# Kernel tuning notes

Hardware: AMD Instinct MI355X
Metric: run time of the kernel (lower is better)

## Reference

```python
import jax, jax.numpy as jnp
import numpy as np

B, T, D, H = 256, 256, 64, 512  # batch, seq_len, input_dim, hidden_dim


def setup_inputs() -> dict:
    key = jax.random.key(0)
    ks = jax.random.split(key, 12)
    scale = 0.05
    inp = {"x": jax.random.normal(ks[0], (B, T, D), dtype=jnp.float32)}
    in_dims = [D, H, H]
    for i in range(3):
        inp[f"Wx{i}"] = jax.random.normal(ks[1 + 3 * i], (in_dims[i], H), dtype=jnp.float32) * scale
        inp[f"Wh{i}"] = jax.random.normal(ks[2 + 3 * i], (H, H), dtype=jnp.float32) * scale
        inp[f"b{i}"] = jnp.zeros((H,), dtype=jnp.float32)
    inp["Wf"] = jax.random.normal(ks[10], (H, 1), dtype=jnp.float32) * scale
    inp["bf"] = jnp.zeros((1,), dtype=jnp.float32)
    return inp


def _rnn_seq(x, Wx, Wh, b):
    """SimpleRNN with return_sequences=True. x: [B,T,Din] -> [B,T,H].
    Keras eval mode: dropout inactive. h_t = tanh(x_t Wx + h_{t-1} Wh + b)."""
    # Precompute input projection for all steps (one big GEMM).
    xp = jnp.einsum('btd,dh->bth', x, Wx) + b  # [B,T,H]

    def step(h, xt):
        h2 = jnp.tanh(xt + h @ Wh)
        return h2, h2

    h0 = jnp.zeros((x.shape[0], Wh.shape[0]), dtype=x.dtype)
    _, ys = jax.lax.scan(step, h0, jnp.swapaxes(xp, 0, 1))  # ys: [T,B,H]
    return jnp.swapaxes(ys, 0, 1)


def _rnn_last(x, Wx, Wh, b):
    """SimpleRNN with return_sequences=False. x: [B,T,Din] -> [B,H] (final state)."""
    xp = jnp.einsum('btd,dh->bth', x, Wx) + b

    def step(h, xt):
        h2 = jnp.tanh(xt + h @ Wh)
        return h2, None

    h0 = jnp.zeros((x.shape[0], Wh.shape[0]), dtype=x.dtype)
    hT, _ = jax.lax.scan(step, h0, jnp.swapaxes(xp, 0, 1))
    return hT


def reference(x, Wx0, Wh0, b0, Wx1, Wh1, b1, Wx2, Wh2, b2, Wf, bf):
    h = _rnn_seq(x, Wx0, Wh0, b0)   # [B,T,H]
    h = _rnn_seq(h, Wx1, Wh1, b1)   # [B,T,H]
    h = _rnn_last(h, Wx2, Wh2, b2)  # [B,H]
    return h @ Wf + bf              # [B,1]
```

## Files before the change

kernel.cpp:

```cpp
#include <hip/hip_runtime.h>


typedef unsigned short u16;
typedef unsigned int   u32;
typedef unsigned long long u64;

typedef __attribute__((ext_vector_type(8))) short short8;
typedef __attribute__((ext_vector_type(4))) float f32x4;
typedef __attribute__((ext_vector_type(4))) int   i32x4;

#define N_B 256
#define N_T 256
#define N_D 64
#define N_H 512
#define LAY 3
#define BG  8
#define CGS 8
#define ROWS 32
#define WCOL 64
#define NWG (LAY * BG * CGS)
#define CNT_TGT 8
#define CPAD 16
#define CNT_LINES (LAY * BG * N_T)
#define XBASE ((CNT_LINES + 2 * BG) * CPAD)
#define XCCS  (XBASE + CPAD)
#define CNT_U32 (XCCS + NWG)
#define SPIN_LIM (1u << 22)

__device__ __forceinline__ u16 f2bf(float f) {
  union { float f; u32 u; } v; v.f = f;
  u32 u = v.u;
  u += 0x7fffu + ((u >> 16) & 1u);
  return (u16)(u >> 16);
}
__device__ __forceinline__ float bf2f(u16 h) {
  union { u32 u; float f; } v; v.u = ((u32)h) << 16;
  return v.f;
}
__device__ __forceinline__ short8 ld8(const u16* p) { return *(const short8*)p; }
__device__ __forceinline__ short8 cvt8(const float* p) {
  short8 r;
#pragma unroll
  for (int j = 0; j < 8; ++j) r[j] = (short)f2bf(p[j]);
  return r;
}
__device__ __forceinline__ short8 as_s8(i32x4 v) {
  union { i32x4 i; short8 s; } u; u.i = v; return u.s;
}
__device__ __forceinline__ float fast_tanh(float x) {
  float xc = fminf(fmaxf(x, -9.f), 9.f);
  float e  = __builtin_amdgcn_exp2f(xc * 2.8853900817779268f);
  return 1.f - 2.f * __builtin_amdgcn_rcpf(e + 1.f);
}
__device__ __forceinline__ u32 rmw_read(u32* p) {
  u32 v, z = 0;
  asm volatile("global_atomic_add %0, %1, %2, off sc0\n\ts_waitcnt vmcnt(0)"
               : "=v"(v) : "v"(p), "v"(z) : "memory");
  return v;
}
__device__ __forceinline__ void poll_cnt(u32* cp, u32 target, bool fast, bool* dead) {
  u32 it = 0;
  for (;;) {
    u32 v = fast ? rmw_read(cp)
                 : __hip_atomic_load(cp, __ATOMIC_RELAXED, __HIP_MEMORY_SCOPE_AGENT);
    if (v >= target) return;
    if (it >= 2) __builtin_amdgcn_s_sleep(1);
    if (++it > SPIN_LIM) { *dead = true; return; }
  }
}
__device__ __forceinline__ void lds_set(volatile u32* f, u32 v) {
  __hip_atomic_store((u32*)f, v, __ATOMIC_RELEASE, __HIP_MEMORY_SCOPE_WORKGROUP);
}
__device__ __forceinline__ void lds_wait(volatile u32* f, u32 want, bool* dead) {
  u32 it = 0;
  while (__hip_atomic_load((u32*)f, __ATOMIC_ACQUIRE, __HIP_MEMORY_SCOPE_WORKGROUP) != want) {
    if (++it > SPIN_LIM) { *dead = true; return; }
  }
}

__device__ __forceinline__ void load16_async_fast(const u16* p, i32x4 f[16]) {
  asm volatile(
      "global_load_dwordx4 %0, %16, off sc0\n\t"
      "global_load_dwordx4 %1, %16, off offset:64 sc0\n\t"
      "global_load_dwordx4 %2, %16, off offset:128 sc0\n\t"
      "global_load_dwordx4 %3, %16, off offset:192 sc0\n\t"
      "global_load_dwordx4 %4, %16, off offset:256 sc0\n\t"
      "global_load_dwordx4 %5, %16, off offset:320 sc0\n\t"
      "global_load_dwordx4 %6, %16, off offset:384 sc0\n\t"
      "global_load_dwordx4 %7, %16, off offset:448 sc0\n\t"
      "global_load_dwordx4 %8, %16, off offset:512 sc0\n\t"
      "global_load_dwordx4 %9, %16, off offset:576 sc0\n\t"
      "global_load_dwordx4 %10, %16, off offset:640 sc0\n\t"
      "global_load_dwordx4 %11, %16, off offset:704 sc0\n\t"
      "global_load_dwordx4 %12, %16, off offset:768 sc0\n\t"
      "global_load_dwordx4 %13, %16, off offset:832 sc0\n\t"
      "global_load_dwordx4 %14, %16, off offset:896 sc0\n\t"
      "global_load_dwordx4 %15, %16, off offset:960 sc0"
      : "=&v"(f[0]), "=&v"(f[1]), "=&v"(f[2]), "=&v"(f[3]),
        "=&v"(f[4]), "=&v"(f[5]), "=&v"(f[6]), "=&v"(f[7]),
        "=&v"(f[8]), "=&v"(f[9]), "=&v"(f[10]), "=&v"(f[11]),
        "=&v"(f[12]), "=&v"(f[13]), "=&v"(f[14]), "=&v"(f[15])
      : "v"(p) : "memory");
}
__device__ __forceinline__ void load16_async_slow(const u16* p, i32x4 f[16]) {
  asm volatile(
      "global_load_dwordx4 %0, %16, off sc0 sc1\n\t"
      "global_load_dwordx4 %1, %16, off offset:64 sc0 sc1\n\t"
      "global_load_dwordx4 %2, %16, off offset:128 sc0 sc1\n\t"
      "global_load_dwordx4 %3, %16, off offset:192 sc0 sc1\n\t"
      "global_load_dwordx4 %4, %16, off offset:256 sc0 sc1\n\t"
      "global_load_dwordx4 %5, %16, off offset:320 sc0 sc1\n\t"
      "global_load_dwordx4 %6, %16, off offset:384 sc0 sc1\n\t"
      "global_load_dwordx4 %7, %16, off offset:448 sc0 sc1\n\t"
      "global_load_dwordx4 %8, %16, off offset:512 sc0 sc1\n\t"
      "global_load_dwordx4 %9, %16, off offset:576 sc0 sc1\n\t"
      "global_load_dwordx4 %10, %16, off offset:640 sc0 sc1\n\t"
      "global_load_dwordx4 %11, %16, off offset:704 sc0 sc1\n\t"
      "global_load_dwordx4 %12, %16, off offset:768 sc0 sc1\n\t"
      "global_load_dwordx4 %13, %16, off offset:832 sc0 sc1\n\t"
      "global_load_dwordx4 %14, %16, off offset:896 sc0 sc1\n\t"
      "global_load_dwordx4 %15, %16, off offset:960 sc0 sc1"
      : "=&v"(f[0]), "=&v"(f[1]), "=&v"(f[2]), "=&v"(f[3]),
        "=&v"(f[4]), "=&v"(f[5]), "=&v"(f[6]), "=&v"(f[7]),
        "=&v"(f[8]), "=&v"(f[9]), "=&v"(f[10]), "=&v"(f[11]),
        "=&v"(f[12]), "=&v"(f[13]), "=&v"(f[14]), "=&v"(f[15])
      : "v"(p) : "memory");
}

#define MFMA16(a, b, c) __builtin_amdgcn_mfma_f32_16x16x32_bf16((a), (b), (c), 0, 0, 0)

#define STEPK(kt, N)                                                        \
  do {                                                                      \
    asm volatile("s_waitcnt vmcnt(" #N ")" : "+v"(fr[kt]) :: "memory");     \
    short8 a_ = as_s8(fr[kt]);                                              \
    acc[0] = MFMA16(a_, wf[kt][0], acc[0]);                                 \
    acc[1] = MFMA16(a_, wf[kt][1], acc[1]);                                 \
    acc[2] = MFMA16(a_, wf[kt][2], acc[2]);                                 \
    acc[3] = MFMA16(a_, wf[kt][3], acc[3]);                                 \
  } while (0)
#define K16_PIPE()                                                          \
  STEPK(0, 15); STEPK(1, 14); STEPK(2, 13); STEPK(3, 12);                   \
  STEPK(4, 11); STEPK(5, 10); STEPK(6, 9);  STEPK(7, 8);                    \
  STEPK(8, 7);  STEPK(9, 6);  STEPK(10, 5); STEPK(11, 4);                   \
  STEPK(12, 3); STEPK(13, 2); STEPK(14, 1); STEPK(15, 0)

__global__ __launch_bounds__(256, 1)
void rnn_pipe(const float* __restrict__ x,
              const float* __restrict__ Wx0, const float* __restrict__ Wh0, const float* __restrict__ b0,
              const float* __restrict__ Wx1, const float* __restrict__ Wh1, const float* __restrict__ b1,
              const float* __restrict__ Wx2, const float* __restrict__ Wh2, const float* __restrict__ b2,
              u16* __restrict__ seq0, u16* __restrict__ seq1, u16* __restrict__ seq2,
              u32* __restrict__ cnt) {
  const int tid  = threadIdx.x;
  const int lane = tid & 63;
  const int w    = tid >> 6;
  const int quad = lane >> 4;
  const int l16  = lane & 15;
  const int half = w & 1;
  const bool is_rec = (w < 2);

  __shared__ u16   WhT[WCOL][N_H];
  __shared__ u16   WxT[WCOL][N_H];
  __shared__ float Cbuf[2][ROWS][WCOL + 1];
  __shared__ u32   sflags[6];
  __shared__ u32   sx[NWG];
  __shared__ u32   sbar;

  u32* arrive = cnt + XBASE;
  u32* xccs   = cnt + XCCS;

  u32 xcc;
  asm volatile("s_getreg_b32 %0, hwreg(HW_REG_XCC_ID)" : "=s"(xcc));
  if (tid == 0) {
    u32* xe = xccs + blockIdx.x;
    u32 xv = xcc & 7u;
    asm volatile("global_store_dword %0, %1, off sc0 sc1\n\ts_waitcnt vmcnt(0)"
                 :: "v"(xe), "v"(xv) : "memory");
    __hip_atomic_fetch_add(arrive, 1u, __ATOMIC_RELAXED, __HIP_MEMORY_SCOPE_AGENT);
    u32 it = 0; u32 bd = 0;
    while (rmw_read(arrive) < (u32)NWG) {
      __builtin_amdgcn_s_sleep(1);
      if (++it > SPIN_LIM) { bd = 1; break; }
    }
    sbar = bd;
  }
  if (tid < 6) sflags[tid] = 0;
  __syncthreads();
  const bool bar_dead = (sbar != 0);
  if (!bar_dead && tid < NWG) sx[tid] = rmw_read(xccs + tid) & 7u;
  __syncthreads();

  int bg, layer, j; bool fast;
  if (bar_dead) {
    bg = blockIdx.x & 7;
    int rst = blockIdx.x >> 3;
    layer = rst >> 3; j = rst & 7;
    fast = false;
  } else {
    u64 c64 = 0;
    int myrid = -1, mypend = -1, pends = 0;
    for (int i = 0; i < NWG; ++i) {
      u32 xv = sx[i];
      u32 c = (u32)((c64 >> (8u * xv)) & 0xffu);
      if (c < 24u) {
        if (i == (int)blockIdx.x) myrid = (int)(xv * 24u + c);
        c64 += (1ull << (8u * xv));
      } else {
        if (i == (int)blockIdx.x) mypend = pends;
        ++pends;
      }
    }
    if (myrid < 0) {
      int p = 0;
      for (int xb = 0; xb < 8; ++xb) {
        u32 c = (u32)((c64 >> (8u * xb)) & 0xffu);
        for (u32 s = c; s < 24u; ++s) {
          if (p == mypend) myrid = xb * 24 + (int)s;
          ++p;
        }
      }
    }
    bg = myrid / 24;
    int slot = myrid % 24;
    layer = slot >> 3; j = slot & 7;
    fast = (((c64 >> (8u * (u32)bg)) & 0xffu) >= 24u);
  }
  const int b = bg;

  const float *Wx, *Wh, *bias; const u16 *in_seq = nullptr; u16 *out_seq;
  if (layer == 0)      { Wx = Wx0; Wh = Wh0; bias = b0; out_seq = seq0; }
  else if (layer == 1) { Wx = Wx1; Wh = Wh1; bias = b1; in_seq = seq0; out_seq = seq1; }
  else                 { Wx = Wx2; Wh = Wh2; bias = b2; in_seq = seq1; out_seq = seq2; }
  const int kin = (layer == 0) ? N_D : N_H;
  u32* cnt_own  = cnt + (size_t)(layer * BG + b) * N_T * CPAD;
  u32* cnt_prev = (layer > 0) ? cnt + (size_t)((layer - 1) * BG + b) * N_T * CPAD : nullptr;

  for (int e = tid; e < WCOL * N_H; e += 256) {
    int n = e & 63, k = e >> 6;
    WhT[n][(k + 8 * n) & (N_H - 1)] = f2bf(Wh[k * N_H + j * WCOL + n]);
  }
  for (int e = tid; e < WCOL * kin; e += 256) {
    int n = e & 63, k = e >> 6;
    WxT[n][(k + 8 * n) & (kin - 1)] = f2bf(Wx[k * N_H + j * WCOL + n]);
  }
  float bv[4];
#pragma unroll
  for (int n = 0; n < 4; ++n) bv[n] = bias[j * WCOL + n * 16 + l16];
  __syncthreads();

  short8 wf[16][4];
  if (is_rec) {
#pragma unroll
    for (int kt = 0; kt < 16; ++kt)
#pragma unroll
      for (int n = 0; n < 4; ++n) {
        int nl = n * 16 + l16;
        wf[kt][n] = ld8(&WhT[nl][(kt * 32 + quad * 8 + 8 * nl) & (N_H - 1)]);
      }
  } else if (layer == 0) {
#pragma unroll
    for (int n = 0; n < 4; ++n) {
      int nl = n * 16 + l16;
      wf[0][n] = ld8(&WxT[nl][(quad * 8 + 8 * nl) & (N_D - 1)]);
      wf[1][n] = ld8(&WxT[nl][(32 + quad * 8 + 8 * nl) & (N_D - 1)]);
    }
  } else {
#pragma unroll
    for (int kt = 0; kt < 16; ++kt)
#pragma unroll
      for (int n = 0; n < 4; ++n) {
        int nl = n * 16 + l16;
        wf[kt][n] = ld8(&WxT[nl][(kt * 32 + quad * 8 + 8 * nl) & (N_H - 1)]);
      }
  }

  const int arow = b * ROWS + half * 16 + l16;
  bool dead = false;

  for (int t = 0; t < N_T; ++t) {
    const int par = t & 1;
    f32x4 acc[4] = {{0.f,0.f,0.f,0.f},{0.f,0.f,0.f,0.f},{0.f,0.f,0.f,0.f},{0.f,0.f,0.f,0.f}};

    if (!is_rec) {
      if (layer == 0) {
        const float* xp = x + ((size_t)arow * N_T + t) * N_D + quad * 8;
        short8 f0 = cvt8(xp), f1 = cvt8(xp + 32);
#pragma unroll
        for (int n = 0; n < 4; ++n) {
          acc[n] = MFMA16(f0, wf[0][n], acc[n]);
          acc[n] = MFMA16(f1, wf[1][n], acc[n]);
        }
      } else {
        if (half == 0) {
          if (lane == 0) {
            if (!dead) poll_cnt(cnt_prev + (size_t)t * CPAD, CNT_TGT, fast, &dead);
            lds_set(&sflags[2 + par], (u32)(t + 1));
          }
        } else {
          if (lane == 0 && !dead) lds_wait(&sflags[2 + par], (u32)(t + 1), &dead);
        }
        const u16* sp = in_seq + ((size_t)t * N_B + arow) * N_H + quad * 8;
        i32x4 fr[16];
        if (fast) load16_async_fast(sp, fr);
        else      load16_async_slow(sp, fr);
        K16_PIPE();
      }
      int rb = half * 16 + quad * 4;
#pragma unroll
      for (int n = 0; n < 4; ++n)
#pragma unroll
        for (int r = 0; r < 4; ++r)
          Cbuf[par][rb + r][n * 16 + l16] = acc[n][r];
    } else {
      if (t > 0) {
        if (half == 0) {
          if (lane == 0) {
            if (!dead) poll_cnt(cnt_own + (size_t)(t - 1) * CPAD, CNT_TGT, fast, &dead);
            lds_set(&sflags[par], (u32)t);
          }
        } else {
          if (lane == 0 && !dead) lds_wait(&sflags[par], (u32)t, &dead);
        }
        const u16* ap = out_seq + ((size_t)(t - 1) * N_B + arow) * N_H + quad * 8;
        i32x4 fr[16];
        if (fast) load16_async_fast(ap, fr);
        else      load16_async_slow(ap, fr);
        K16_PIPE();
      }
    }

    __syncthreads();

    if (is_rec) {
      int rb = half * 16 + quad * 4;
      u32 hv[4][4];
#pragma unroll
      for (int n = 0; n < 4; ++n)
#pragma unroll
        for (int r = 0; r < 4; ++r)
          hv[n][r] = (u32)f2bf(fast_tanh(acc[n][r] + Cbuf[par][rb + r][n * 16 + l16] + bv[n]));
      u16* hdst = out_seq + ((size_t)t * N_B + b * ROWS + half * 16 + quad * 4) * N_H
                  + j * WCOL + l16;
      if (fast) {
        asm volatile(
            "global_store_short %0, %1, off sc0\n\t"
            "global_store_short %0, %2, off offset:1024 sc0\n\t"
            "global_store_short %0, %3, off offset:2048 sc0\n\t"
            "global_store_short %0, %4, off offset:3072 sc0\n\t"
            "global_store_short %0, %5, off offset:32 sc0\n\t"
            "global_store_short %0, %6, off offset:1056 sc0\n\t"
            "global_store_short %0, %7, off offset:2080 sc0\n\t"
            "global_store_short %0, %8, off offset:3104 sc0\n\t"
            "global_store_short %0, %9, off offset:64 sc0\n\t"
            "global_store_short %0, %10, off offset:1088 sc0\n\t"
            "global_store_short %0, %11, off offset:2112 sc0\n\t"
            "global_store_short %0, %12, off offset:3136 sc0\n\t"
            "global_store_short %0, %13, off offset:96 sc0\n\t"
            "global_store_short %0, %14, off offset:1120 sc0\n\t"
            "global_store_short %0, %15, off offset:2144 sc0\n\t"
            "global_store_short %0, %16, off offset:3168 sc0"
            :: "v"(hdst),
               "v"(hv[0][0]), "v"(hv[0][1]), "v"(hv[0][2]), "v"(hv[0][3]),
               "v"(hv[1][0]), "v"(hv[1][1]), "v"(hv[1][2]), "v"(hv[1][3]),
               "v"(hv[2][0]), "v"(hv[2][1]), "v"(hv[2][2]), "v"(hv[2][3]),
               "v"(hv[3][0]), "v"(hv[3][1]), "v"(hv[3][2]), "v"(hv[3][3])
            : "memory");
      } else {
        asm volatile(
            "global_store_short %0, %1, off sc0 sc1\n\t"
            "global_store_short %0, %2, off offset:1024 sc0 sc1\n\t"
            "global_store_short %0, %3, off offset:2048 sc0 sc1\n\t"
            "global_store_short %0, %4, off offset:3072 sc0 sc1\n\t"
            "global_store_short %0, %5, off offset:32 sc0 sc1\n\t"
            "global_store_short %0, %6, off offset:1056 sc0 sc1\n\t"
            "global_store_short %0, %7, off offset:2080 sc0 sc1\n\t"
            "global_store_short %0, %8, off offset:3104 sc0 sc1\n\t"
            "global_store_short %0, %9, off offset:64 sc0 sc1\n\t"
            "global_store_short %0, %10, off offset:1088 sc0 sc1\n\t"
            "global_store_short %0, %11, off offset:2112 sc0 sc1\n\t"
            "global_store_short %0, %12, off offset:3136 sc0 sc1\n\t"
            "global_store_short %0, %13, off offset:96 sc0 sc1\n\t"
            "global_store_short %0, %14, off offset:1120 sc0 sc1\n\t"
            "global_store_short %0, %15, off offset:2144 sc0 sc1\n\t"
            "global_store_short %0, %16, off offset:3168 sc0 sc1"
            :: "v"(hdst),
               "v"(hv[0][0]), "v"(hv[0][1]), "v"(hv[0][2]), "v"(hv[0][3]),
               "v"(hv[1][0]), "v"(hv[1][1]), "v"(hv[1][2]), "v"(hv[1][3]),
               "v"(hv[2][0]), "v"(hv[2][1]), "v"(hv[2][2]), "v"(hv[2][3]),
               "v"(hv[3][0]), "v"(hv[3][1]), "v"(hv[3][2]), "v"(hv[3][3])
            : "memory");
      }
      asm volatile("s_waitcnt vmcnt(0)" ::: "memory");
      if (half == 1) {
        if (lane == 0) lds_set(&sflags[4 + par], (u32)(t + 1));
      } else {
        if (lane == 0) {
          if (!dead) lds_wait(&sflags[4 + par], (u32)(t + 1), &dead);
          u32* cp = cnt_own + (size_t)t * CPAD;
          if (fast) {
            u32 one = 1u;
            asm volatile("global_atomic_add %0, %1, off" :: "v"(cp), "v"(one) : "memory");
          } else {
            __hip_atomic_fetch_add(cp, 1u, __ATOMIC_RELAXED, __HIP_MEMORY_SCOPE_AGENT);
          }
        }
      }
    }
  }
}

__global__ void head_kernel(const u16* __restrict__ seq2, const float* __restrict__ Wf,
                            const float* __restrict__ bf, float* __restrict__ out) {
  int b    = blockIdx.x;
  int lane = threadIdx.x;
  const u16* hrow = seq2 + ((size_t)(N_T - 1) * N_B + b) * N_H;
  float s = 0.f;
#pragma unroll
  for (int r = 0; r < N_H / 64; ++r) {
    int idx = lane * 8 + r;
    s += bf2f(hrow[idx]) * Wf[idx];
  }
#pragma unroll
  for (int off = 32; off > 0; off >>= 1) s += __shfl_down(s, off);
  if (lane == 0) out[b] = s + bf[0];
}

extern "C" void kernel_launch(void* const* d_in, const int* in_sizes, int n_in,
                              void* d_out, int out_size, void* d_ws, size_t ws_size,
                              hipStream_t stream) {
  const float* x   = (const float*)d_in[0];
  const float* Wx0 = (const float*)d_in[1];
  const float* Wh0 = (const float*)d_in[2];
  const float* b0  = (const float*)d_in[3];
  const float* Wx1 = (const float*)d_in[4];
  const float* Wh1 = (const float*)d_in[5];
  const float* b1  = (const float*)d_in[6];
  const float* Wx2 = (const float*)d_in[7];
  const float* Wh2 = (const float*)d_in[8];
  const float* b2  = (const float*)d_in[9];
  const float* Wf  = (const float*)d_in[10];
  const float* bf  = (const float*)d_in[11];
  float* out = (float*)d_out;

  const size_t SEQ_BYTES = (size_t)N_T * N_B * N_H * sizeof(u16);
  if (ws_size < 3 * SEQ_BYTES + (size_t)CNT_U32 * sizeof(u32)) return;

  char* ws  = (char*)d_ws;
  u16* seq0 = (u16*)(ws);
  u16* seq1 = (u16*)(ws + SEQ_BYTES);
  u16* seq2 = (u16*)(ws + 2 * SEQ_BYTES);
  u32* cnt  = (u32*)(ws + 3 * SEQ_BYTES);

  (void)hipMemsetAsync(cnt, 0, (size_t)CNT_U32 * sizeof(u32), stream);

  rnn_pipe<<<LAY * BG * CGS, 256, 0, stream>>>(x, Wx0, Wh0, b0, Wx1, Wh1, b1,
                                               Wx2, Wh2, b2, seq0, seq1, seq2,
                                               cnt);
  head_kernel<<<N_B, 64, 0, stream>>>(seq2, Wf, bf, out);
}
```

Before: 1.079 ms.

## Replace per-timestep shared counters with per-workgroup monotonic step counters polled by 8 lanes

Cross-workgroup step signalling moves from one shared atomic counter per (layer, batch group, timestep) that eight producers increment to one monotonic counter line per producer workgroup. Consumers have eight lanes each poll one producer's line and use a wave-wide all-vote to decide readiness. The aim is to remove atomic contention on a single line and to shrink the counter footprint from per-timestep lines to a fixed set. The cost is eight parallel polls per wait instead of one. Correctness relies on each counter being monotonic and visible to the polling lanes.

```diff
diff --git a/kernel.cpp b/kernel.cpp
--- a/kernel.cpp
+++ b/kernel.cpp
@@ -19,11 +19,10 @@
 #define ROWS 32
 #define WCOL 64
 #define NWG (LAY * BG * CGS)
-#define CNT_TGT 8
 #define CPAD 16
-#define CNT_LINES (LAY * BG * N_T)
-#define XBASE ((CNT_LINES + 2 * BG) * CPAD)
-#define XCCS  (XBASE + CPAD)
+#define STEP_U32 (LAY * BG * CGS * CPAD)
+#define XBASE  STEP_U32
+#define XCCS   (XBASE + CPAD)
 #define CNT_U32 (XCCS + NWG)
 #define SPIN_LIM (1u << 22)
 
@@ -58,13 +57,24 @@
                : "=v"(v) : "v"(p), "v"(z) : "memory");
   return v;
 }
-__device__ __forceinline__ void poll_cnt(u32* cp, u32 target, bool fast, bool* dead) {
+__device__ __forceinline__ void poll8(u32* base, u32 tgt, bool fast, bool* dead, int lane) {
+  u32* lp = base + (size_t)(lane & 7) * CPAD;
+  const bool active = (lane < 8);
   u32 it = 0;
   for (;;) {
-    u32 v = fast ? rmw_read(cp)
-                 : __hip_atomic_load(cp, __ATOMIC_RELAXED, __HIP_MEMORY_SCOPE_AGENT);
-    if (v >= target) return;
+    u32 v = tgt;
+    if (active)
+      v = fast ? rmw_read(lp)
+               : __hip_atomic_load(lp, __ATOMIC_RELAXED, __HIP_MEMORY_SCOPE_AGENT);
+    if (__all((int)(v >= tgt))) return;
     if (it >= 2) __builtin_amdgcn_s_sleep(1);
+    if (++it > SPIN_LIM) { *dead = true; return; }
+  }
+}
+__device__ __forceinline__ void poll_one(u32* cp, u32 target, bool* dead) {
+  u32 it = 0;
+  while (rmw_read(cp) < target) {
+    __builtin_amdgcn_s_sleep(1);
     if (++it > SPIN_LIM) { *dead = true; return; }
   }
 }
@@ -177,12 +187,9 @@
     asm volatile("global_store_dword %0, %1, off sc0 sc1\n\ts_waitcnt vmcnt(0)"
                  :: "v"(xe), "v"(xv) : "memory");
     __hip_atomic_fetch_add(arrive, 1u, __ATOMIC_RELAXED, __HIP_MEMORY_SCOPE_AGENT);
-    u32 it = 0; u32 bd = 0;
-    while (rmw_read(arrive) < (u32)NWG) {
-      __builtin_amdgcn_s_sleep(1);
-      if (++it > SPIN_LIM) { bd = 1; break; }
-    }
-    sbar = bd;
+    bool bd = false;
+    poll_one(arrive, (u32)NWG, &bd);
+    sbar = bd ? 1u : 0u;
   }
   if (tid < 6) sflags[tid] = 0;
   __syncthreads();
@@ -232,8 +239,9 @@
   else if (layer == 1) { Wx = Wx1; Wh = Wh1; bias = b1; in_seq = seq0; out_seq = seq1; }
   else                 { Wx = Wx2; Wh = Wh2; bias = b2; in_seq = seq1; out_seq = seq2; }
   const int kin = (layer == 0) ? N_D : N_H;
-  u32* cnt_own  = cnt + (size_t)(layer * BG + b) * N_T * CPAD;
-  u32* cnt_prev = (layer > 0) ? cnt + (size_t)((layer - 1) * BG + b) * N_T * CPAD : nullptr;
+  u32* own_base  = cnt + (size_t)((layer * BG + b) * CGS) * CPAD;
+  u32* prev_base = (layer > 0) ? cnt + (size_t)(((layer - 1) * BG + b) * CGS) * CPAD : nullptr;
+  u32* own_line  = own_base + (size_t)j * CPAD;
 
   for (int e = tid; e < WCOL * N_H; e += 256) {
     int n = e & 63, k = e >> 6;
@@ -292,10 +300,8 @@
         }
       } else {
         if (half == 0) {
-          if (lane == 0) {
-            if (!dead) poll_cnt(cnt_prev + (size_t)t * CPAD, CNT_TGT, fast, &dead);
-            lds_set(&sflags[2 + par], (u32)(t + 1));
-          }
+          if (!dead) poll8(prev_base, (u32)(t + 1), fast, &dead, lane);
+          if (lane == 0) lds_set(&sflags[2 + par], (u32)(t + 1));
         } else {
           if (lane == 0 && !dead) lds_wait(&sflags[2 + par], (u32)(t + 1), &dead);
         }
@@ -314,10 +320,8 @@
     } else {
       if (t > 0) {
         if (half == 0) {
-          if (lane == 0) {
-            if (!dead) poll_cnt(cnt_own + (size_t)(t - 1) * CPAD, CNT_TGT, fast, &dead);
-            lds_set(&sflags[par], (u32)t);
-          }
+          if (!dead) poll8(own_base, (u32)t, fast, &dead, lane);
+          if (lane == 0) lds_set(&sflags[par], (u32)t);
         } else {
           if (lane == 0 && !dead) lds_wait(&sflags[par], (u32)t, &dead);
         }
@@ -396,12 +400,11 @@
       } else {
         if (lane == 0) {
           if (!dead) lds_wait(&sflags[4 + par], (u32)(t + 1), &dead);
-          u32* cp = cnt_own + (size_t)t * CPAD;
           if (fast) {
             u32 one = 1u;
-            asm volatile("global_atomic_add %0, %1, off" :: "v"(cp), "v"(one) : "memory");
+            asm volatile("global_atomic_add %0, %1, off" :: "v"(own_line), "v"(one) : "memory");
           } else {
-            __hip_atomic_fetch_add(cp, 1u, __ATOMIC_RELAXED, __HIP_MEMORY_SCOPE_AGENT);
+            __hip_atomic_fetch_add(own_line, 1u, __ATOMIC_RELAXED, __HIP_MEMORY_SCOPE_AGENT);
           }
         }
       }
```

After: 1.117 ms. +3.5%, slower.
